# Kernel tuning notes

Measured on AMD Instinct MI355X. Metric: run time of the kernel, lower is better.

Reference implementation:

```python
import jax, jax.numpy as jnp
import numpy as np

EPS = 1e-5

def _layer_norm(x, w, b):
    mu = jnp.mean(x, axis=-1, keepdims=True)
    var = jnp.mean((x - mu) ** 2, axis=-1, keepdims=True)
    return (x - mu) * jax.lax.rsqrt(var + EPS) * w + b

def setup_inputs() -> dict:
    H = 2048
    B, T = 4, 2048
    key = jax.random.key(0)
    ks = jax.random.split(key, 12)
    s = 0.02
    return {
        "hidden_state": jax.random.normal(ks[0], (B, T, H), dtype=jnp.float32),
        "ln_w": jnp.ones((H,), jnp.float32),
        "ln_b": jnp.zeros((H,), jnp.float32),
        "Wk": jax.random.normal(ks[1], (H, H), jnp.float32) * s,
        "Wv": jax.random.normal(ks[2], (H, H), jnp.float32) * s,
        "Wr": jax.random.normal(ks[3], (H, H), jnp.float32) * s,
        "Wo": jax.random.normal(ks[4], (H, H), jnp.float32) * s,
        "mix_k": jax.random.uniform(ks[5], (H,), jnp.float32),
        "mix_v": jax.random.uniform(ks[6], (H,), jnp.float32),
        "mix_r": jax.random.uniform(ks[7], (H,), jnp.float32),
        "time_decay": jax.random.normal(ks[8], (H,), jnp.float32) * 0.5,
        "current_token_weight": jax.random.normal(ks[9], (H,), jnp.float32) * 0.5,
    }

def _wkv(k, v, time_decay, curr_w):
    # k, v: [B, T, H]; max-stabilized RWKV recurrence, scanned over time.
    B, T, H = k.shape
    decay = -jnp.exp(time_decay)  # [H]
    num0 = jnp.zeros((B, H), k.dtype)
    den0 = jnp.zeros((B, H), k.dtype)
    norm0 = jnp.full((B, H), -jnp.inf, k.dtype)

    def step(carry, kv):
        num, den, norm = carry
        kt, vt = kv  # [B, H]
        ct = curr_w + kt
        cn = jnp.maximum(ct, norm)
        e_prev = jnp.exp(norm - cn)
        e_cur = jnp.exp(ct - cn)
        out = (e_prev * num + e_cur * vt) / (e_prev * den + e_cur)
        dpn = decay + norm
        new_norm = jnp.maximum(dpn, kt)
        e_d = jnp.exp(dpn - new_norm)
        e_k = jnp.exp(kt - new_norm)
        return (e_d * num + e_k * vt, e_d * den + e_k, new_norm), out

    kT = jnp.swapaxes(k, 0, 1)  # [T, B, H]
    vT = jnp.swapaxes(v, 0, 1)
    (num, den, norm), outs = jax.lax.scan(step, (num0, den0, norm0), (kT, vT))
    return jnp.swapaxes(outs, 0, 1), num, den, norm

def reference(hidden_state, ln_w, ln_b, Wk, Wv, Wr, Wo, mix_k, mix_v, mix_r,
              time_decay, current_token_weight):
    residual = hidden_state
    x = _layer_norm(hidden_state, ln_w, ln_b)  # [B, T, H]
    B, T, H = x.shape
    # shifted input: previous token (zeros for t=0 since previous_state is None)
    sx = jnp.concatenate([jnp.zeros((B, 1, H), x.dtype), x[:, :-1, :]], axis=1)
    xk = sx + mix_k * (x - sx)
    xv = sx + mix_v * (x - sx)
    xr = sx + mix_r * (x - sx)
    r = jax.nn.sigmoid(jnp.einsum('bth,oh->bto', xr, Wr))
    k = jnp.einsum('bth,oh->bto', xk, Wk)
    v = jnp.einsum('bth,oh->bto', xv, Wv)
    wkv, num, den, norm = _wkv(k, v, time_decay, current_token_weight)
    rwkv = jnp.einsum('bth,oh->bto', r * wkv, Wo)
    out = residual + rwkv
    return (out, (x[:, -1, :], num, den, norm))
```

## Files before the change

kernel.cpp:

```cpp
#include <hip/hip_runtime.h>
#include <hip/hip_bf16.h>
#include <stdint.h>

#define B_ 4
#define T_ 2048
#define H_ 2048
#define BT_ (B_ * T_)
#define BH_ (B_ * H_)
#define CH_ 32
#define CL_ (T_ / CH_)
#define NT_ (H_ / 32)

typedef __bf16 bf16x8 __attribute__((ext_vector_type(8)));
typedef float f32x4 __attribute__((ext_vector_type(4)));

__device__ inline void async16(const void* g, void* l) {
  __builtin_amdgcn_global_load_lds(
      (__attribute__((address_space(1))) uint32_t*)(void*)(uintptr_t)g,
      (__attribute__((address_space(3))) uint32_t*)l,
      16, 0, 0);
}

__global__ __launch_bounds__(256) void cvt_bf16_kernel(
    const float* __restrict__ src, __bf16* __restrict__ dst) {
  int i = (blockIdx.x * 256 + threadIdx.x) * 8;
  const float4* s4 = (const float4*)(src + i);
  float4 a = s4[0], b = s4[1];
  bf16x8 o;
  o[0] = (__bf16)a.x; o[1] = (__bf16)a.y; o[2] = (__bf16)a.z; o[3] = (__bf16)a.w;
  o[4] = (__bf16)b.x; o[5] = (__bf16)b.y; o[6] = (__bf16)b.z; o[7] = (__bf16)b.w;
  *(bf16x8*)(dst + i) = o;
}

__global__ __launch_bounds__(256) void ln_mix_kernel(
    const float* __restrict__ h, const float* __restrict__ lnw,
    const float* __restrict__ lnb, const float* __restrict__ mk,
    const float* __restrict__ mv, const float* __restrict__ mr,
    __bf16* __restrict__ xk, __bf16* __restrict__ xv, __bf16* __restrict__ xr,
    float* __restrict__ xlast) {
  const int row = blockIdx.x;
  const int t = row & (T_ - 1);
  const int tid = threadIdx.x;
  const bool hasprev = (t != 0);

  const float4* cr = (const float4*)(h + (size_t)row * H_);
  float4 c0 = cr[tid * 2 + 0], c1 = cr[tid * 2 + 1];
  float4 p0 = {0.f, 0.f, 0.f, 0.f}, p1 = {0.f, 0.f, 0.f, 0.f};
  if (hasprev) {
    const float4* pr = (const float4*)(h + (size_t)(row - 1) * H_);
    p0 = pr[tid * 2 + 0]; p1 = pr[tid * 2 + 1];
  }
  float4 red;
  red.x = c0.x + c0.y + c0.z + c0.w + c1.x + c1.y + c1.z + c1.w;
  red.y = c0.x * c0.x + c0.y * c0.y + c0.z * c0.z + c0.w * c0.w +
          c1.x * c1.x + c1.y * c1.y + c1.z * c1.z + c1.w * c1.w;
  red.z = p0.x + p0.y + p0.z + p0.w + p1.x + p1.y + p1.z + p1.w;
  red.w = p0.x * p0.x + p0.y * p0.y + p0.z * p0.z + p0.w * p0.w +
          p1.x * p1.x + p1.y * p1.y + p1.z * p1.z + p1.w * p1.w;
  #pragma unroll
  for (int off = 32; off; off >>= 1) {
    red.x += __shfl_down(red.x, off);
    red.y += __shfl_down(red.y, off);
    red.z += __shfl_down(red.z, off);
    red.w += __shfl_down(red.w, off);
  }
  __shared__ float4 rbuf[4];
  const int lane = tid & 63, wid = tid >> 6;
  if (lane == 0) rbuf[wid] = red;
  __syncthreads();
  float4 tot;
  tot.x = rbuf[0].x + rbuf[1].x + rbuf[2].x + rbuf[3].x;
  tot.y = rbuf[0].y + rbuf[1].y + rbuf[2].y + rbuf[3].y;
  tot.z = rbuf[0].z + rbuf[1].z + rbuf[2].z + rbuf[3].z;
  tot.w = rbuf[0].w + rbuf[1].w + rbuf[2].w + rbuf[3].w;

  const float inv = 1.0f / (float)H_;
  float mu = tot.x * inv;
  float rstd = rsqrtf(fmaxf(tot.y * inv - mu * mu, 0.f) + 1e-5f);
  float mup = tot.z * inv;
  float rstdp = rsqrtf(fmaxf(tot.w * inv - mup * mup, 0.f) + 1e-5f);

  float xc[8] = {c0.x, c0.y, c0.z, c0.w, c1.x, c1.y, c1.z, c1.w};
  float xp[8] = {p0.x, p0.y, p0.z, p0.w, p1.x, p1.y, p1.z, p1.w};
  const float4* W4 = (const float4*)lnw;
  const float4* Bv4 = (const float4*)lnb;
  const float4* MK4 = (const float4*)mk;
  const float4* MV4 = (const float4*)mv;
  const float4* MR4 = (const float4*)mr;
  float4 w0 = W4[tid * 2], w1 = W4[tid * 2 + 1];
  float4 b0 = Bv4[tid * 2], b1 = Bv4[tid * 2 + 1];
  float4 k0 = MK4[tid * 2], k1 = MK4[tid * 2 + 1];
  float4 v0 = MV4[tid * 2], v1 = MV4[tid * 2 + 1];
  float4 r0 = MR4[tid * 2], r1 = MR4[tid * 2 + 1];
  float wa[8] = {w0.x, w0.y, w0.z, w0.w, w1.x, w1.y, w1.z, w1.w};
  float ba[8] = {b0.x, b0.y, b0.z, b0.w, b1.x, b1.y, b1.z, b1.w};
  float ka[8] = {k0.x, k0.y, k0.z, k0.w, k1.x, k1.y, k1.z, k1.w};
  float va[8] = {v0.x, v0.y, v0.z, v0.w, v1.x, v1.y, v1.z, v1.w};
  float ra[8] = {r0.x, r0.y, r0.z, r0.w, r1.x, r1.y, r1.z, r1.w};

  bf16x8 ok_, ov_, or_;
  float xls[8];
  #pragma unroll
  for (int e = 0; e < 8; e++) {
    float x = (xc[e] - mu) * rstd * wa[e] + ba[e];
    float sx = hasprev ? (xp[e] - mup) * rstdp * wa[e] + ba[e] : 0.f;
    ok_[e] = (__bf16)(sx + ka[e] * (x - sx));
    ov_[e] = (__bf16)(sx + va[e] * (x - sx));
    or_[e] = (__bf16)(sx + ra[e] * (x - sx));
    xls[e] = x;
  }
  size_t obase = (size_t)row * H_ + tid * 8;
  *(bf16x8*)(xk + obase) = ok_;
  *(bf16x8*)(xv + obase) = ov_;
  *(bf16x8*)(xr + obase) = or_;
  if (t == T_ - 1) {
    float* dst = xlast + (size_t)(row >> 11) * H_ + tid * 8;
    #pragma unroll
    for (int e = 0; e < 8; e++) dst[e] = xls[e];
  }
}


__device__ inline void stage_pair(const char* Ab, const char* Bb, char* slotbase,
                                  int kt, int pair, int wv, int lane) {
  const char* Mb = pair ? Bb : Ab;
  #pragma unroll
  for (int hlf = 0; hlf < 2; hlf++) {
    int r = pair * 2 + hlf;
    char* dst = slotbase + r * 8192 + wv * 1024;
    int row = hlf * 128 + wv * 16 + (lane >> 2);
    const char* src = Mb + (size_t)row * (H_ * 2) + kt * 64 + (lane & 3) * 16;
    async16(src, dst);
  }
}

template <int MODE>
__global__ __launch_bounds__(512, 2) void gemm_nt2(
    const __bf16* __restrict__ A, const __bf16* __restrict__ Bw,
    float* __restrict__ outf, __bf16* __restrict__ outb,
    const float* __restrict__ resid) {
  __shared__ __align__(16) char ring[4][32768];

  const int wgid = blockIdx.x;
  const int lin = (wgid & 7) * 32 + (wgid >> 3);
  const int bm = lin >> 3;
  const int bn = lin & 7;

  const int tid = threadIdx.x;
  const int lane = tid & 63, wv = tid >> 6;
  const int wm = wv >> 2;
  const int wn = wv & 3;
  const int rr = lane & 15, q = lane >> 4;

  f32x4 acc[8][4];
  #pragma unroll
  for (int m = 0; m < 8; m++)
    #pragma unroll
    for (int n = 0; n < 4; n++) acc[m][n] = (f32x4){0.f, 0.f, 0.f, 0.f};

  const char* Ab = (const char*)A + (size_t)bm * 256 * (H_ * 2);
  const char* Bb = (const char*)Bw + (size_t)bn * 256 * (H_ * 2);

  stage_pair(Ab, Bb, ring[0], 0, 0, wv, lane);
  stage_pair(Ab, Bb, ring[0], 0, 1, wv, lane);
  stage_pair(Ab, Bb, ring[1], 1, 0, wv, lane);
  stage_pair(Ab, Bb, ring[1], 1, 1, wv, lane);
  asm volatile("s_waitcnt vmcnt(4)" ::: "memory");
  __builtin_amdgcn_s_barrier();

  for (int kt = 0; kt < NT_; kt++) {
    const __bf16* Alds = (const __bf16*)(ring[kt & 3]);
    const __bf16* Blds = (const __bf16*)(ring[kt & 3] + 16384);
    char* nslot = ring[(kt + 2) & 3];
    const bool pf = (kt + 2 < NT_);

    bf16x8 af[4], bfr[4];
    #pragma unroll
    for (int mi = 0; mi < 4; mi++)
      af[mi] = *(const bf16x8*)(Alds + (size_t)(wm * 128 + mi * 16 + rr) * 32 + q * 8);
    #pragma unroll
    for (int ni = 0; ni < 4; ni++)
      bfr[ni] = *(const bf16x8*)(Blds + (size_t)(wn * 64 + ni * 16 + rr) * 32 + q * 8);
    if (pf) stage_pair(Ab, Bb, nslot, kt + 2, 0, wv, lane);
    __builtin_amdgcn_sched_barrier(0);
    __builtin_amdgcn_s_barrier();
    __builtin_amdgcn_sched_barrier(0);
    __builtin_amdgcn_s_setprio(1);
    #pragma unroll
    for (int mi = 0; mi < 4; mi++)
      #pragma unroll
      for (int ni = 0; ni < 4; ni++)
        acc[mi][ni] = __builtin_amdgcn_mfma_f32_16x16x32_bf16(af[mi], bfr[ni], acc[mi][ni], 0, 0, 0);
    __builtin_amdgcn_s_setprio(0);
    __builtin_amdgcn_sched_barrier(0);
    __builtin_amdgcn_s_barrier();
    __builtin_amdgcn_sched_barrier(0);

    #pragma unroll
    for (int mi = 0; mi < 4; mi++)
      af[mi] = *(const bf16x8*)(Alds + (size_t)(wm * 128 + 64 + mi * 16 + rr) * 32 + q * 8);
    if (pf) stage_pair(Ab, Bb, nslot, kt + 2, 1, wv, lane);
    if (kt < NT_ - 2) {
      asm volatile("s_waitcnt vmcnt(4)" ::: "memory");
    } else {
      asm volatile("s_waitcnt vmcnt(0)" ::: "memory");
    }
    __builtin_amdgcn_sched_barrier(0);
    __builtin_amdgcn_s_barrier();
    __builtin_amdgcn_sched_barrier(0);
    __builtin_amdgcn_s_setprio(1);
    #pragma unroll
    for (int mi = 0; mi < 4; mi++)
      #pragma unroll
      for (int ni = 0; ni < 4; ni++)
        acc[4 + mi][ni] = __builtin_amdgcn_mfma_f32_16x16x32_bf16(af[mi], bfr[ni], acc[4 + mi][ni], 0, 0, 0);
    __builtin_amdgcn_s_setprio(0);
    __builtin_amdgcn_sched_barrier(0);
    __builtin_amdgcn_s_barrier();
    __builtin_amdgcn_sched_barrier(0);
  }

  const int r0 = bm * 256 + wm * 128 + q * 4;
  const int c0 = bn * 256 + wn * 64 + rr;
  #pragma unroll
  for (int m = 0; m < 8; m++) {
    #pragma unroll
    for (int n = 0; n < 4; n++) {
      int col = c0 + n * 16;
      #pragma unroll
      for (int rg = 0; rg < 4; rg++) {
        int rowg = r0 + m * 16 + rg;
        size_t idx = (size_t)rowg * H_ + col;
        float vv = acc[m][n][rg];
        if (MODE == 0) {
          outf[idx] = vv;
        } else if (MODE == 1) {
          outb[idx] = (__bf16)(1.f / (1.f + __expf(-vv)));
        } else {
          outf[idx] = resid[idx] + vv;
        }
      }
    }
  }
}

__global__ __launch_bounds__(256) void wkv_pass1(
    const float* __restrict__ k, const float* __restrict__ v,
    const float* __restrict__ td,
    float* __restrict__ cs_num, float* __restrict__ cs_den,
    float* __restrict__ cs_norm) {
  const int id = blockIdx.x * 256 + threadIdx.x;
  const int c = blockIdx.y;
  const int b = id >> 11;
  const int hh = id & (H_ - 1);
  const float decay = -__expf(td[hh]);
  float num = 0.f, den = 0.f, norm = -INFINITY;

  const int UN = 16;
  for (int t0 = c * CL_; t0 < (c + 1) * CL_; t0 += UN) {
    float kk[UN], vv[UN];
    size_t base = ((size_t)b * T_ + t0) * H_ + hh;
    #pragma unroll
    for (int i = 0; i < UN; i++) {
      kk[i] = k[base + (size_t)i * H_];
      vv[i] = v[base + (size_t)i * H_];
    }
    #pragma unroll
    for (int i = 0; i < UN; i++) {
      float dpn = decay + norm;
      float nn = fmaxf(dpn, kk[i]);
      float ed = __expf(dpn - nn), ek = __expf(kk[i] - nn);
      num = ed * num + ek * vv[i];
      den = ed * den + ek;
      norm = nn;
    }
  }
  cs_num[c * BH_ + id] = num;
  cs_den[c * BH_ + id] = den;
  cs_norm[c * BH_ + id] = norm;
}

__global__ __launch_bounds__(256) void wkv_scan(
    const float* __restrict__ cs_num, const float* __restrict__ cs_den,
    const float* __restrict__ cs_norm, const float* __restrict__ td,
    float* __restrict__ px_num, float* __restrict__ px_den,
    float* __restrict__ px_norm) {
  const int id = blockIdx.x * 256 + threadIdx.x;
  const int hh = id & (H_ - 1);
  const float Lw = -__expf(td[hh]) * (float)CL_;
  float num = 0.f, den = 0.f, norm = -INFINITY;
  for (int c = 0; c < CH_; c++) {
    px_num[c * BH_ + id] = num;
    px_den[c * BH_ + id] = den;
    px_norm[c * BH_ + id] = norm;
    float n_c = cs_num[c * BH_ + id];
    float d_c = cs_den[c * BH_ + id];
    float m_c = cs_norm[c * BH_ + id];
    float sn = norm + Lw;
    float on = fmaxf(sn, m_c);
    float ea = __expf(sn - on), eb = __expf(m_c - on);
    num = ea * num + eb * n_c;
    den = ea * den + eb * d_c;
    norm = on;
  }
}

__global__ __launch_bounds__(256) void wkv_pass2(
    const float* __restrict__ k, const float* __restrict__ v,
    const __bf16* __restrict__ r, const float* __restrict__ td,
    const float* __restrict__ cw,
    const float* __restrict__ px_num, const float* __restrict__ px_den,
    const float* __restrict__ px_norm,
    __bf16* __restrict__ a, float* __restrict__ ndn) {
  const int id = blockIdx.x * 256 + threadIdx.x;
  const int c = blockIdx.y;
  const int b = id >> 11;
  const int hh = id & (H_ - 1);
  const float decay = -__expf(td[hh]);
  const float cwv = cw[hh];
  float num = px_num[c * BH_ + id];
  float den = px_den[c * BH_ + id];
  float norm = px_norm[c * BH_ + id];

  const int UN = 16;
  for (int t0 = c * CL_; t0 < (c + 1) * CL_; t0 += UN) {
    float kk[UN], vv[UN], rrv[UN];
    size_t base = ((size_t)b * T_ + t0) * H_ + hh;
    #pragma unroll
    for (int i = 0; i < UN; i++) {
      kk[i] = k[base + (size_t)i * H_];
      vv[i] = v[base + (size_t)i * H_];
      rrv[i] = (float)r[base + (size_t)i * H_];
    }
    #pragma unroll
    for (int i = 0; i < UN; i++) {
      float kt = kk[i], vt = vv[i];
      float ct = cwv + kt;
      float cn = fmaxf(ct, norm);
      float ep = __expf(norm - cn), ec = __expf(ct - cn);
      float o = (ep * num + ec * vt) / (ep * den + ec);
      a[base + (size_t)i * H_] = (__bf16)(rrv[i] * o);
      float dpn = decay + norm;
      float nn = fmaxf(dpn, kt);
      float ed = __expf(dpn - nn), ek = __expf(kt - nn);
      num = ed * num + ek * vt;
      den = ed * den + ek;
      norm = nn;
    }
  }
  if (c == CH_ - 1) {
    ndn[id] = num;
    ndn[BH_ + id] = den;
    ndn[2 * BH_ + id] = norm;
  }
}

extern "C" void kernel_launch(void* const* d_in, const int* in_sizes, int n_in,
                              void* d_out, int out_size, void* d_ws, size_t ws_size,
                              hipStream_t stream) {
  const float* h   = (const float*)d_in[0];
  const float* lnw = (const float*)d_in[1];
  const float* lnb = (const float*)d_in[2];
  const float* Wk  = (const float*)d_in[3];
  const float* Wv  = (const float*)d_in[4];
  const float* Wr  = (const float*)d_in[5];
  const float* Wo  = (const float*)d_in[6];
  const float* mk  = (const float*)d_in[7];
  const float* mv  = (const float*)d_in[8];
  const float* mr  = (const float*)d_in[9];
  const float* td  = (const float*)d_in[10];
  const float* cw  = (const float*)d_in[11];

  char* ws = (char*)d_ws;
  const size_t MB = 1048576;
  __bf16* xk   = (__bf16*)(ws);
  __bf16* xv   = (__bf16*)(ws + 32 * MB);
  __bf16* xr   = (__bf16*)(ws + 64 * MB);
  float*  kbuf = (float*)(ws + 96 * MB);
  float*  vbuf = (float*)(ws + 160 * MB);
  __bf16* Wk16 = (__bf16*)(ws + 224 * MB);
  __bf16* Wv16 = Wk16 + (size_t)H_ * H_;
  __bf16* Wr16 = Wv16 + (size_t)H_ * H_;
  __bf16* Wo16 = Wr16 + (size_t)H_ * H_;
  float* cs_num  = (float*)(ws + 64 * MB);
  float* cs_den  = cs_num + (size_t)CH_ * BH_;
  float* cs_norm = cs_den + (size_t)CH_ * BH_;
  float* px_num  = cs_norm + (size_t)CH_ * BH_;
  float* px_den  = px_num + (size_t)CH_ * BH_;
  float* px_norm = px_den + (size_t)CH_ * BH_;

  float* out  = (float*)d_out;
  float* xlast = out + (size_t)BT_ * H_;
  float* ndn   = xlast + (size_t)B_ * H_;

  const int cvt_blocks = (H_ * H_) / (256 * 8);
  cvt_bf16_kernel<<<cvt_blocks, 256, 0, stream>>>(Wk, Wk16);
  cvt_bf16_kernel<<<cvt_blocks, 256, 0, stream>>>(Wv, Wv16);
  cvt_bf16_kernel<<<cvt_blocks, 256, 0, stream>>>(Wr, Wr16);
  cvt_bf16_kernel<<<cvt_blocks, 256, 0, stream>>>(Wo, Wo16);

  ln_mix_kernel<<<BT_, 256, 0, stream>>>(h, lnw, lnb, mk, mv, mr, xk, xv, xr, xlast);

  const int gemm_blocks = (BT_ / 256) * (H_ / 256);
  gemm_nt2<0><<<gemm_blocks, 512, 0, stream>>>(xk, Wk16, kbuf, nullptr, nullptr);
  gemm_nt2<0><<<gemm_blocks, 512, 0, stream>>>(xv, Wv16, vbuf, nullptr, nullptr);
  gemm_nt2<1><<<gemm_blocks, 512, 0, stream>>>(xr, Wr16, nullptr, xv , nullptr);

  dim3 wg(BH_ / 256, CH_);
  wkv_pass1<<<wg, 256, 0, stream>>>(kbuf, vbuf, td, cs_num, cs_den, cs_norm);
  wkv_scan<<<BH_ / 256, 256, 0, stream>>>(cs_num, cs_den, cs_norm, td,
                                          px_num, px_den, px_norm);
  wkv_pass2<<<wg, 256, 0, stream>>>(kbuf, vbuf, xv, td, cw,
                                    px_num, px_den, px_norm,
                                    xk , ndn);

  gemm_nt2<2><<<gemm_blocks, 512, 0, stream>>>(xk, Wo16, out, nullptr, h);
}
```

Measured before the change: 434.6 us.

## Rework GEMM main loop to K=64 tiles with swizzled LDS and double buffering

Measured after the change: 429.6 us. Within noise of the previous version (-1.2%).

```diff
diff --git a/kernel.cpp b/kernel.cpp
--- a/kernel.cpp
+++ b/kernel.cpp
@@ -9,7 +9,7 @@
 #define BH_ (B_ * H_)
 #define CH_ 32
 #define CL_ (T_ / CH_)
-#define NT_ (H_ / 32)
+#define NKT_ (H_ / 64)
 
 typedef __bf16 bf16x8 __attribute__((ext_vector_type(8)));
 typedef float f32x4 __attribute__((ext_vector_type(4)));
@@ -120,26 +120,12 @@
   }
 }
 
-
-__device__ inline void stage_pair(const char* Ab, const char* Bb, char* slotbase,
-                                  int kt, int pair, int wv, int lane) {
-  const char* Mb = pair ? Bb : Ab;
-  #pragma unroll
-  for (int hlf = 0; hlf < 2; hlf++) {
-    int r = pair * 2 + hlf;
-    char* dst = slotbase + r * 8192 + wv * 1024;
-    int row = hlf * 128 + wv * 16 + (lane >> 2);
-    const char* src = Mb + (size_t)row * (H_ * 2) + kt * 64 + (lane & 3) * 16;
-    async16(src, dst);
-  }
-}
-
 template <int MODE>
-__global__ __launch_bounds__(512, 2) void gemm_nt2(
+__global__ __launch_bounds__(512, 1) void gemm_nt3(
     const __bf16* __restrict__ A, const __bf16* __restrict__ Bw,
     float* __restrict__ outf, __bf16* __restrict__ outb,
     const float* __restrict__ resid) {
-  __shared__ __align__(16) char ring[4][32768];
+  __shared__ __align__(16) char ring[2][65536];
 
   const int wgid = blockIdx.x;
   const int lin = (wgid & 7) * 32 + (wgid >> 3);
@@ -158,67 +144,88 @@
     #pragma unroll
     for (int n = 0; n < 4; n++) acc[m][n] = (f32x4){0.f, 0.f, 0.f, 0.f};
 
-  const char* Ab = (const char*)A + (size_t)bm * 256 * (H_ * 2);
-  const char* Bb = (const char*)Bw + (size_t)bn * 256 * (H_ * 2);
-
-  stage_pair(Ab, Bb, ring[0], 0, 0, wv, lane);
-  stage_pair(Ab, Bb, ring[0], 0, 1, wv, lane);
-  stage_pair(Ab, Bb, ring[1], 1, 0, wv, lane);
-  stage_pair(Ab, Bb, ring[1], 1, 1, wv, lane);
-  asm volatile("s_waitcnt vmcnt(4)" ::: "memory");
+  const char* Ag = (const char*)A + (size_t)(bm * 256) * (H_ * 2);
+  const char* Bg = (const char*)Bw + (size_t)(bn * 256) * (H_ * 2);
+
+  const int srow = wv * 8 + (lane >> 3);
+  const int scol = ((lane & 7) ^ (lane >> 3)) << 4;
+
+  const int rsw = rr & 7;
+
+#define STAGE_TILE(kt_, buf_)                                                   \
+  {                                                                             \
+    char* base_ = ring[buf_];                                                   \
+    _Pragma("unroll")                                                           \
+    for (int mh_ = 0; mh_ < 2; mh_++) {                                         \
+      const char* Mg_ = mh_ ? Bg : Ag;                                          \
+      _Pragma("unroll")                                                         \
+      for (int hh_ = 0; hh_ < 2; hh_++) {                                       \
+        _Pragma("unroll")                                                       \
+        for (int rd_ = 0; rd_ < 2; rd_++) {                                     \
+          char* dst_ = base_ + mh_ * 32768 + hh_ * 16384 + rd_ * 8192 + wv * 1024; \
+          const char* src_ = Mg_ + (size_t)(hh_ * 128 + rd_ * 64 + srow) * (H_ * 2) \
+                             + (kt_) * 128 + scol;                              \
+          async16(src_, dst_);                                                  \
+        }                                                                       \
+      }                                                                         \
+    }                                                                           \
+  }
+
+  STAGE_TILE(0, 0);
+  asm volatile("s_waitcnt vmcnt(0)" ::: "memory");
   __builtin_amdgcn_s_barrier();
 
-  for (int kt = 0; kt < NT_; kt++) {
-    const __bf16* Alds = (const __bf16*)(ring[kt & 3]);
-    const __bf16* Blds = (const __bf16*)(ring[kt & 3] + 16384);
-    char* nslot = ring[(kt + 2) & 3];
-    const bool pf = (kt + 2 < NT_);
-
-    bf16x8 af[4], bfr[4];
-    #pragma unroll
-    for (int mi = 0; mi < 4; mi++)
-      af[mi] = *(const bf16x8*)(Alds + (size_t)(wm * 128 + mi * 16 + rr) * 32 + q * 8);
-    #pragma unroll
-    for (int ni = 0; ni < 4; ni++)
-      bfr[ni] = *(const bf16x8*)(Blds + (size_t)(wn * 64 + ni * 16 + rr) * 32 + q * 8);
-    if (pf) stage_pair(Ab, Bb, nslot, kt + 2, 0, wv, lane);
-    __builtin_amdgcn_sched_barrier(0);
-    __builtin_amdgcn_s_barrier();
-    __builtin_amdgcn_sched_barrier(0);
-    __builtin_amdgcn_s_setprio(1);
-    #pragma unroll
-    for (int mi = 0; mi < 4; mi++)
+  bf16x8 bfr[4][2];
+
+  for (int kt = 0; kt < NKT_; kt++) {
+    const int cur = kt & 1, nxt = cur ^ 1;
+    const char* Alds = ring[cur];
+    const char* Blds = ring[cur] + 32768;
+
+    #pragma unroll
+    for (int p = 0; p < 4; p++) {
+      if (p == 0) {
+        #pragma unroll
+        for (int ni = 0; ni < 4; ni++)
+          #pragma unroll
+          for (int ks = 0; ks < 2; ks++) {
+            int row_t = wn * 64 + ni * 16 + rr;
+            bfr[ni][ks] = *(const bf16x8*)(Blds + row_t * 128 +
+                                           (((ks * 4 + q) ^ rsw) << 4));
+          }
+      }
+      bf16x8 af[2][2];
       #pragma unroll
-      for (int ni = 0; ni < 4; ni++)
-        acc[mi][ni] = __builtin_amdgcn_mfma_f32_16x16x32_bf16(af[mi], bfr[ni], acc[mi][ni], 0, 0, 0);
-    __builtin_amdgcn_s_setprio(0);
-    __builtin_amdgcn_sched_barrier(0);
-    __builtin_amdgcn_s_barrier();
-    __builtin_amdgcn_sched_barrier(0);
-
-    #pragma unroll
-    for (int mi = 0; mi < 4; mi++)
-      af[mi] = *(const bf16x8*)(Alds + (size_t)(wm * 128 + 64 + mi * 16 + rr) * 32 + q * 8);
-    if (pf) stage_pair(Ab, Bb, nslot, kt + 2, 1, wv, lane);
-    if (kt < NT_ - 2) {
-      asm volatile("s_waitcnt vmcnt(4)" ::: "memory");
-    } else {
-      asm volatile("s_waitcnt vmcnt(0)" ::: "memory");
-    }
-    __builtin_amdgcn_sched_barrier(0);
-    __builtin_amdgcn_s_barrier();
-    __builtin_amdgcn_sched_barrier(0);
-    __builtin_amdgcn_s_setprio(1);
-    #pragma unroll
-    for (int mi = 0; mi < 4; mi++)
+      for (int mi = 0; mi < 2; mi++)
+        #pragma unroll
+        for (int ks = 0; ks < 2; ks++) {
+          int row_t = wm * 128 + p * 32 + mi * 16 + rr;
+          af[mi][ks] = *(const bf16x8*)(Alds + row_t * 128 +
+                                        (((ks * 4 + q) ^ rsw) << 4));
+        }
+      if (p == 0 && kt + 1 < NKT_) STAGE_TILE(kt + 1, nxt);
+      if (p == 3) asm volatile("s_waitcnt vmcnt(0)" ::: "memory");
+      __builtin_amdgcn_sched_barrier(0);
+      __builtin_amdgcn_s_barrier();
+      __builtin_amdgcn_sched_barrier(0);
+      asm volatile("s_waitcnt lgkmcnt(0)" ::: "memory");
+      __builtin_amdgcn_sched_barrier(0);
+      __builtin_amdgcn_s_setprio(1);
       #pragma unroll
-      for (int ni = 0; ni < 4; ni++)
-        acc[4 + mi][ni] = __builtin_amdgcn_mfma_f32_16x16x32_bf16(af[mi], bfr[ni], acc[4 + mi][ni], 0, 0, 0);
-    __builtin_amdgcn_s_setprio(0);
-    __builtin_amdgcn_sched_barrier(0);
-    __builtin_amdgcn_s_barrier();
-    __builtin_amdgcn_sched_barrier(0);
-  }
+      for (int ks = 0; ks < 2; ks++)
+        #pragma unroll
+        for (int mi = 0; mi < 2; mi++)
+          #pragma unroll
+          for (int ni = 0; ni < 4; ni++)
+            acc[p * 2 + mi][ni] = __builtin_amdgcn_mfma_f32_16x16x32_bf16(
+                af[mi][ks], bfr[ni][ks], acc[p * 2 + mi][ni], 0, 0, 0);
+      __builtin_amdgcn_s_setprio(0);
+      __builtin_amdgcn_sched_barrier(0);
+      __builtin_amdgcn_s_barrier();
+      __builtin_amdgcn_sched_barrier(0);
+    }
+  }
+#undef STAGE_TILE
 
   const int r0 = bm * 256 + wm * 128 + q * 4;
   const int c0 = bn * 256 + wn * 64 + rr;
@@ -402,9 +409,9 @@
   ln_mix_kernel<<<BT_, 256, 0, stream>>>(h, lnw, lnb, mk, mv, mr, xk, xv, xr, xlast);
 
   const int gemm_blocks = (BT_ / 256) * (H_ / 256);
-  gemm_nt2<0><<<gemm_blocks, 512, 0, stream>>>(xk, Wk16, kbuf, nullptr, nullptr);
-  gemm_nt2<0><<<gemm_blocks, 512, 0, stream>>>(xv, Wv16, vbuf, nullptr, nullptr);
-  gemm_nt2<1><<<gemm_blocks, 512, 0, stream>>>(xr, Wr16, nullptr, xv , nullptr);
+  gemm_nt3<0><<<gemm_blocks, 512, 0, stream>>>(xk, Wk16, kbuf, nullptr, nullptr);
+  gemm_nt3<0><<<gemm_blocks, 512, 0, stream>>>(xv, Wv16, vbuf, nullptr, nullptr);
+  gemm_nt3<1><<<gemm_blocks, 512, 0, stream>>>(xr, Wr16, nullptr, xv , nullptr);
 
   dim3 wg(BH_ / 256, CH_);
   wkv_pass1<<<wg, 256, 0, stream>>>(kbuf, vbuf, td, cs_num, cs_den, cs_norm);
@@ -414,5 +421,5 @@
                                     px_num, px_den, px_norm,
                                     xk , ndn);
 
-  gemm_nt2<2><<<gemm_blocks, 512, 0, stream>>>(xk, Wo16, out, nullptr, h);
-}
+  gemm_nt3<2><<<gemm_blocks, 512, 0, stream>>>(xk, Wo16, out, nullptr, h);
+}
```
